# Optimization experiments

Hardware: AMD Instinct MI355X
Metric: run time of the kernel (lower is better)

Reference implementation:

```python
import jax, jax.numpy as jnp
import numpy as np

B, L, D, H, W = 32, 1024, 512, 8, 5  # batch, seq, d_model, heads, local_context_length
DK = D // H


def _local_mix(x, W0, b0, w):
    """Sliding-window local-context weighting (faithful to the torch loop version).
    Pads front with w-1 zeros, applies linear (so padded rows become the bias),
    softmax-weights each length-w causal window against the current position,
    and sums the window.  x: [B, L, D] -> [B, L, D]."""
    Bb, Ll, Dd = x.shape
    xp = jnp.pad(x, ((0, 0), (w - 1, 0), (0, 0)))          # [B, L+w-1, D]
    xp = xp @ W0 + b0                                       # linear AFTER pad (padded rows = bias)
    idx = jnp.arange(Ll)[:, None] + jnp.arange(w)[None, :]  # [L, w] window indices into padded seq
    win = xp[:, idx, :]                                     # [B, L, w, D]
    cur = xp[:, w - 1:, :]                                  # [B, L, D] current positions
    scores = jnp.einsum('bld,blwd->blw', cur, win) / jnp.sqrt(jnp.float32(Dd))
    wts = jax.nn.softmax(scores, axis=-1)                   # [B, L, w]
    return jnp.einsum('blw,blwd->bld', wts, win)            # [B, L, D]


def setup_inputs() -> dict:
    rng = jax.random.key(0)
    ks = jax.random.split(rng, 7)
    s = 0.02
    return {
        'query': jax.random.normal(ks[0], (B, L, D), jnp.float32),
        'key':   jax.random.normal(ks[1], (B, L, D), jnp.float32),
        'value': jax.random.normal(ks[2], (B, L, D), jnp.float32),
        'W0':    jax.random.normal(ks[3], (D, D), jnp.float32) * s,
        'b0':    jax.random.normal(ks[4], (D,), jnp.float32) * s,
        'Wout':  jax.random.normal(ks[5], (D, D), jnp.float32) * s,
        'bout':  jax.random.normal(ks[6], (D,), jnp.float32) * s,
    }


def reference(query, key, value, W0, b0, Wout, bout):
    q = _local_mix(query, W0, b0, W).reshape(B, L, H, DK).transpose(0, 2, 1, 3)  # [B,H,L,dk]
    k = _local_mix(key, W0, b0, W).reshape(B, L, H, DK).transpose(0, 2, 1, 3)
    v = (value @ W0 + b0).reshape(B, L, H, DK).transpose(0, 2, 1, 3)
    scores = jnp.einsum('bhqd,bhkd->bhqk', q, k) / jnp.sqrt(jnp.float32(DK))     # [B,H,L,L]
    p = jax.nn.softmax(scores, axis=-1)
    x = jnp.einsum('bhqk,bhkd->bhqd', p, v)
    x = x.transpose(0, 2, 1, 3).reshape(B, L, D)
    return x @ Wout + bout
```

## Files before the change

kernel.cpp:

```cpp
#include <hip/hip_runtime.h>


typedef __attribute__((ext_vector_type(8))) short bf16x8;
typedef __attribute__((ext_vector_type(4))) float f32x4;

#define MFMA16(a, b, c) __builtin_amdgcn_mfma_f32_16x16x32_bf16((a), (b), (c), 0, 0, 0)

static __device__ __forceinline__ float bf2f(unsigned short u) {
  union { unsigned int i; float f; } v; v.i = ((unsigned int)u) << 16; return v.f;
}
static __device__ __forceinline__ unsigned short f2b(float f) {
  union { float fv; unsigned int i; } v; v.fv = f;
  unsigned int u = v.i;
  return (unsigned short)((u + 0x7fffu + ((u >> 16) & 1u)) >> 16);
}
static __device__ __forceinline__ unsigned int cvtpk(float lo, float hi) {
  unsigned int r;
  asm("v_cvt_pk_bf16_f32 %0, %1, %2" : "=v"(r) : "v"(lo), "v"(hi));
  return r;
}
static __device__ __forceinline__ void glds16(const void* g, void* l) {
  __builtin_amdgcn_global_load_lds(
      (const __attribute__((address_space(1))) unsigned int*)g,
      (__attribute__((address_space(3))) unsigned int*)l, 16, 0, 0);
}

__global__ __launch_bounds__(256) void tcast2_k(const float* __restrict__ s0,
                                                unsigned short* __restrict__ d0,
                                                const float* __restrict__ s1,
                                                unsigned short* __restrict__ d1) {
  int i = blockIdx.x * 256 + threadIdx.x;
  const float* s = s0;
  unsigned short* d = d0;
  if (i >= 262144) { i -= 262144; s = s1; d = d1; }
  int k = i >> 9, n = i & 511;
  d[(size_t)n * 512 + k] = f2b(s[(size_t)k * 512 + n]);
}

template <int AMODE, int OUTMODE>
__device__ __forceinline__ void gemm_body(const void* __restrict__ A_,
                                          const unsigned short* __restrict__ BT,
                                          const float* __restrict__ bias,
                                          void* __restrict__ out_, int bm, int bn) {
  constexpr int TSZ = (AMODE == 0) ? 16384 : 8192;
  __shared__ __align__(16) char As[2][TSZ];
  const int tid = threadIdx.x;
  const int w = tid >> 6, l = tid & 63;
  const int lg = l >> 4, lr = l & 15;
  const int wr = w >> 1, wc = w & 1;
  const int rowbase = bm * 128;
  const int colbase = bn * 128 + wc * 64;

  f32x4 acc[4][4];
#pragma unroll
  for (int m = 0; m < 4; ++m)
#pragma unroll
    for (int n = 0; n < 4; ++n) acc[m][n] = (f32x4){0.f, 0.f, 0.f, 0.f};

  auto stage = [&](int kt, int buf) {
    if constexpr (AMODE == 0) {
      const float* Af = (const float*)A_;
#pragma unroll
      for (int j = 0; j < 4; ++j) {
        const int rb = w * 32 + j * 8;
        const int r = rb + (l >> 3);
        const int gsrc = (l & 7) ^ (r & 7);
        glds16(Af + (size_t)(rowbase + r) * 512 + kt * 32 + gsrc * 4,
               &As[buf][rb * 128]);
      }
    } else {
      const unsigned short* Ab = (const unsigned short*)A_;
#pragma unroll
      for (int j = 0; j < 2; ++j) {
        const int rb = w * 32 + j * 16;
        const int r = rb + (l >> 2);
        const int gsrc = (l & 3) ^ (r & 3) ^ ((r >> 2) & 3);
        glds16(Ab + (size_t)(rowbase + r) * 512 + kt * 32 + gsrc * 8,
               &As[buf][rb * 64]);
      }
    }
  };

  stage(0, 0);
  __syncthreads();

  for (int kt = 0; kt < 16; ++kt) {
    const int cur = kt & 1;
    bf16x8 bf[4];
#pragma unroll
    for (int n = 0; n < 4; ++n)
      bf[n] = *(const bf16x8*)(BT + (size_t)(colbase + n * 16 + lr) * 512 + kt * 32 + lg * 8);
    if (kt < 15) stage(kt + 1, cur ^ 1);
    bf16x8 af[4];
#pragma unroll
    for (int m = 0; m < 4; ++m) {
      const int r = wr * 64 + m * 16 + lr;
      if constexpr (AMODE == 0) {
        const char* Ro = &As[cur][r * 128];
        const int x = r & 7;
        const float4 a0 = *(const float4*)(Ro + ((((2 * lg) ^ x)) << 4));
        const float4 a1 = *(const float4*)(Ro + ((((2 * lg + 1) ^ x)) << 4));
        union { uint4 d; bf16x8 v; } u;
        u.d.x = cvtpk(a0.x, a0.y); u.d.y = cvtpk(a0.z, a0.w);
        u.d.z = cvtpk(a1.x, a1.y); u.d.w = cvtpk(a1.z, a1.w);
        af[m] = u.v;
      } else {
        const int gsw = lg ^ (r & 3) ^ ((r >> 2) & 3);
        af[m] = *(const bf16x8*)(&As[cur][r * 64 + (gsw << 4)]);
      }
    }
    __builtin_amdgcn_s_setprio(1);
#pragma unroll
    for (int m = 0; m < 4; ++m)
#pragma unroll
      for (int n = 0; n < 4; ++n) acc[m][n] = MFMA16(af[m], bf[n], acc[m][n]);
    __builtin_amdgcn_s_setprio(0);
    __syncthreads();
  }

#pragma unroll
  for (int m = 0; m < 4; ++m)
#pragma unroll
    for (int n = 0; n < 4; ++n) {
      const int grow0 = rowbase + wr * 64 + m * 16 + 4 * lg;
      const int gcol = colbase + n * 16 + lr;
      const float bs = bias[gcol];
#pragma unroll
      for (int r = 0; r < 4; ++r) {
        float v = acc[m][n][r] + bs;
        if constexpr (OUTMODE == 0)
          ((unsigned short*)out_)[(size_t)(grow0 + r) * 512 + gcol] = f2b(v);
        else
          ((float*)out_)[(size_t)(grow0 + r) * 512 + gcol] = v;
      }
    }
}

__global__ __launch_bounds__(256) void proj3_k(const float* __restrict__ q,
                                               const float* __restrict__ k,
                                               const float* __restrict__ v,
                                               const unsigned short* __restrict__ W0T,
                                               const float* __restrict__ b0,
                                               unsigned short* __restrict__ Pq,
                                               unsigned short* __restrict__ Pk,
                                               unsigned short* __restrict__ Pv) {
  const int wg = (blockIdx.x & 7) * 384 + (blockIdx.x >> 3);
  const int t = wg >> 10, rem = wg & 1023;
  const float* A = t == 0 ? q : t == 1 ? k : v;
  unsigned short* O = t == 0 ? Pq : t == 1 ? Pk : Pv;
  gemm_body<0, 0>(A, W0T, b0, O, rem >> 2, rem & 3);
}

__global__ __launch_bounds__(256) void gemmout_k(const unsigned short* __restrict__ A,
                                                 const unsigned short* __restrict__ WoT,
                                                 const float* __restrict__ bout,
                                                 float* __restrict__ out) {
  const int wg = (blockIdx.x & 7) * 128 + (blockIdx.x >> 3);
  gemm_body<1, 1>(A, WoT, bout, out, wg >> 2, wg & 3);
}

__global__ __launch_bounds__(256) void localmix2_k(const unsigned short* __restrict__ Pq,
                                                   const unsigned short* __restrict__ Pk,
                                                   const float* __restrict__ b0,
                                                   unsigned short* __restrict__ Qm,
                                                   unsigned short* __restrict__ Km) {
  const int w = threadIdx.x >> 6, lane = threadIdx.x & 63;
  const int pp = blockIdx.x * 4 + w;
  const unsigned short* P;
  unsigned short* out;
  float outscale;
  int p;
  if (pp < 32768) { P = Pq; out = Qm; outscale = 0.18033688011112042f; p = pp; }
  else            { P = Pk; out = Km; outscale = 1.0f; p = pp - 32768; }
  const int l = p & 1023;
  const int d0 = lane * 8;

  float win[5][8];
#pragma unroll
  for (int j = 0; j < 5; ++j) {
    const int src = l - 4 + j;
    if (src >= 0) {
      const uint4 v = *(const uint4*)(P + (size_t)(p - 4 + j) * 512 + d0);
      const unsigned short* u = (const unsigned short*)&v;
#pragma unroll
      for (int i = 0; i < 8; ++i) win[j][i] = bf2f(u[i]);
    } else {
      const float4 f0 = *(const float4*)(b0 + d0);
      const float4 f1 = *(const float4*)(b0 + d0 + 4);
      win[j][0] = f0.x; win[j][1] = f0.y; win[j][2] = f0.z; win[j][3] = f0.w;
      win[j][4] = f1.x; win[j][5] = f1.y; win[j][6] = f1.z; win[j][7] = f1.w;
    }
  }
  float s[5];
#pragma unroll
  for (int j = 0; j < 5; ++j) {
    float t = 0.f;
#pragma unroll
    for (int i = 0; i < 8; ++i) t += win[4][i] * win[j][i];
    s[j] = t;
  }
#pragma unroll
  for (int off = 1; off < 64; off <<= 1)
#pragma unroll
    for (int j = 0; j < 5; ++j) s[j] += __shfl_xor(s[j], off, 64);
  const float sc = 0.04419417382415922f;
  float mx = -1e30f;
#pragma unroll
  for (int j = 0; j < 5; ++j) { s[j] *= sc; mx = fmaxf(mx, s[j]); }
  float e[5], sum = 0.f;
#pragma unroll
  for (int j = 0; j < 5; ++j) { e[j] = __expf(s[j] - mx); sum += e[j]; }
  const float inv = 1.f / sum;
  __attribute__((ext_vector_type(8))) unsigned short o;
#pragma unroll
  for (int i = 0; i < 8; ++i) {
    float a = 0.f;
#pragma unroll
    for (int j = 0; j < 5; ++j) a += e[j] * win[j][i];
    o[i] = f2b(a * inv * outscale);
  }
  *(__attribute__((ext_vector_type(8))) unsigned short*)(out + (size_t)p * 512 + d0) = o;
}

__global__ __launch_bounds__(256) void attn_k(const unsigned short* __restrict__ Q,
                                              const unsigned short* __restrict__ K,
                                              const unsigned short* __restrict__ V,
                                              unsigned short* __restrict__ AO) {
  __shared__ unsigned short Ks[2][64 * 64];
  __shared__ unsigned short Vt[2][64 * 64];
  const int tid = threadIdx.x;
  const int w = tid >> 6, l = tid & 63;
  const int lg = l >> 4, lr = l & 15;
  const int wg = (blockIdx.x & 7) * 256 + (blockIdx.x >> 3);
  const int qt = wg & 7, bh = wg >> 3;
  const int h = bh & 7, b = bh >> 3;
  const size_t base = (size_t)(b * 1024) * 512 + h * 64;
  const unsigned short* Qb = Q + base + (size_t)(qt * 128) * 512;
  const unsigned short* Kb = K + base;
  const unsigned short* Vb = V + base;

  bf16x8 qf[2][2];
#pragma unroll
  for (int rb = 0; rb < 2; ++rb)
#pragma unroll
    for (int ks = 0; ks < 2; ++ks)
      qf[rb][ks] = *(const bf16x8*)(Qb + (size_t)(w * 32 + rb * 16 + lr) * 512 + ks * 32 + lg * 8);

  f32x4 acc[2][4];
#pragma unroll
  for (int rb = 0; rb < 2; ++rb)
#pragma unroll
    for (int nb = 0; nb < 4; ++nb) acc[rb][nb] = (f32x4){0.f, 0.f, 0.f, 0.f};
  float lrun[2] = {0.f, 0.f};

  const int sk_row = tid >> 2, sk_seg = tid & 3;
  const int sv_key = tid & 63, sv_d0 = (tid >> 6) * 16;
  const int vpos = (sv_key & 32) + ((sv_key >> 2) & 3) * 8 + ((sv_key >> 4) & 1) * 4 + (sv_key & 3);
  const int vpg = vpos >> 3, vpw = vpos & 7;
  const int r7 = sk_row & 7;

  uint4 kr0, kr1, vr0, vr1;
  auto loadT = [&](int t) {
    const uint4* ksrc = (const uint4*)(Kb + (size_t)(t * 64 + sk_row) * 512 + sk_seg * 16);
    kr0 = ksrc[0]; kr1 = ksrc[1];
    const uint4* vsrc = (const uint4*)(Vb + (size_t)(t * 64 + sv_key) * 512 + sv_d0);
    vr0 = vsrc[0]; vr1 = vsrc[1];
  };
  auto writeT = [&](int bufi) {
    unsigned short* kd = Ks[bufi];
    unsigned short* vd = Vt[bufi];
    *(uint4*)&kd[sk_row * 64 + (((2 * sk_seg) ^ r7) << 3)] = kr0;
    *(uint4*)&kd[sk_row * 64 + (((2 * sk_seg + 1) ^ r7) << 3)] = kr1;
    const unsigned short* u0 = (const unsigned short*)&vr0;
    const unsigned short* u1 = (const unsigned short*)&vr1;
#pragma unroll
    for (int j = 0; j < 8; ++j) {
      vd[(sv_d0 + j) * 64 + (((vpg ^ j) << 3) | vpw)] = u0[j];
      vd[(sv_d0 + 8 + j) * 64 + (((vpg ^ j) << 3) | vpw)] = u1[j];
    }
  };

  loadT(0);
  writeT(0);
  loadT(1);
  __syncthreads();

  const int swz0 = (lg ^ (lr & 7)) << 3, swz1 = ((4 + lg) ^ (lr & 7)) << 3;

  for (int it = 0; it < 16; ++it) {
    const int cur = it & 1;
    f32x4 sf[2][4];
    __builtin_amdgcn_s_setprio(1);
#pragma unroll
    for (int kb = 0; kb < 4; ++kb) {
      const int krow = (kb * 16 + lr) * 64;
      bf16x8 kf0 = *(const bf16x8*)&Ks[cur][krow + swz0];
      bf16x8 kf1 = *(const bf16x8*)&Ks[cur][krow + swz1];
#pragma unroll
      for (int rb = 0; rb < 2; ++rb) {
        f32x4 z = (f32x4){0.f, 0.f, 0.f, 0.f};
        z = MFMA16(kf0, qf[rb][0], z);
        z = MFMA16(kf1, qf[rb][1], z);
        sf[rb][kb] = z;
      }
    }
    __builtin_amdgcn_s_setprio(0);

    if (it < 15) writeT((it + 1) & 1);
    if (it < 14) loadT(it + 2);

#pragma unroll
    for (int rb = 0; rb < 2; ++rb) {
#pragma unroll
      for (int kb = 0; kb < 4; ++kb)
#pragma unroll
        for (int r = 0; r < 4; ++r)
          sf[rb][kb][r] = __builtin_amdgcn_exp2f(sf[rb][kb][r]);
      float s0 = (sf[rb][0][0] + sf[rb][0][1]) + (sf[rb][0][2] + sf[rb][0][3]);
      float s1 = (sf[rb][1][0] + sf[rb][1][1]) + (sf[rb][1][2] + sf[rb][1][3]);
      float s2 = (sf[rb][2][0] + sf[rb][2][1]) + (sf[rb][2][2] + sf[rb][2][3]);
      float s3 = (sf[rb][3][0] + sf[rb][3][1]) + (sf[rb][3][2] + sf[rb][3][3]);
      float t = (s0 + s1) + (s2 + s3);
      t += __shfl_xor(t, 16, 64);
      t += __shfl_xor(t, 32, 64);
      lrun[rb] += t;
    }

    union { uint4 d; bf16x8 v; } pa[2][2];
#pragma unroll
    for (int rb = 0; rb < 2; ++rb)
#pragma unroll
      for (int t2 = 0; t2 < 2; ++t2) {
        pa[rb][t2].d.x = cvtpk(sf[rb][2 * t2][0], sf[rb][2 * t2][1]);
        pa[rb][t2].d.y = cvtpk(sf[rb][2 * t2][2], sf[rb][2 * t2][3]);
        pa[rb][t2].d.z = cvtpk(sf[rb][2 * t2 + 1][0], sf[rb][2 * t2 + 1][1]);
        pa[rb][t2].d.w = cvtpk(sf[rb][2 * t2 + 1][2], sf[rb][2 * t2 + 1][3]);
      }

    __builtin_amdgcn_s_setprio(1);
#pragma unroll
    for (int t2 = 0; t2 < 2; ++t2) {
      bf16x8 vf[4];
#pragma unroll
      for (int nb = 0; nb < 4; ++nb) {
        const int vrow = (nb * 16 + lr) * 64;
        vf[nb] = *(const bf16x8*)&Vt[cur][vrow + (((4 * t2 + lg) ^ (lr & 7)) << 3)];
      }
#pragma unroll
      for (int rb = 0; rb < 2; ++rb)
#pragma unroll
        for (int nb = 0; nb < 4; ++nb) acc[rb][nb] = MFMA16(pa[rb][t2].v, vf[nb], acc[rb][nb]);
    }
    __builtin_amdgcn_s_setprio(0);
    if (it < 15) __syncthreads();
  }

#pragma unroll
  for (int rb = 0; rb < 2; ++rb) {
    const float rec = 1.f / lrun[rb];
    float lv[4];
#pragma unroll
    for (int r = 0; r < 4; ++r) lv[r] = __shfl(rec, lg * 4 + r, 64);
#pragma unroll
    for (int nb = 0; nb < 4; ++nb) {
      const int gcol = nb * 16 + lr;
#pragma unroll
      for (int r = 0; r < 4; ++r) {
        const int grow = qt * 128 + w * 32 + rb * 16 + 4 * lg + r;
        AO[base + (size_t)grow * 512 + gcol] = f2b(acc[rb][nb][r] * lv[r]);
      }
    }
  }
}

extern "C" void kernel_launch(void* const* d_in, const int* in_sizes, int n_in,
                              void* d_out, int out_size, void* d_ws, size_t ws_size,
                              hipStream_t stream) {
  const float* query = (const float*)d_in[0];
  const float* key   = (const float*)d_in[1];
  const float* value = (const float*)d_in[2];
  const float* W0    = (const float*)d_in[3];
  const float* b0    = (const float*)d_in[4];
  const float* Wout  = (const float*)d_in[5];
  const float* bout  = (const float*)d_in[6];
  float* out = (float*)d_out;

  char* ws = (char*)d_ws;
  const size_t PSZ = (size_t)32768 * 512 * 2;
  unsigned short* Pq  = (unsigned short*)(ws);
  unsigned short* Pk  = (unsigned short*)(ws + PSZ);
  unsigned short* Pv  = (unsigned short*)(ws + 2 * PSZ);
  unsigned short* Qm  = (unsigned short*)(ws + 3 * PSZ);
  unsigned short* Km  = (unsigned short*)(ws + 4 * PSZ);
  unsigned short* W0T = (unsigned short*)(ws + 5 * PSZ);
  unsigned short* WoT = (unsigned short*)(ws + 5 * PSZ + 524288);

  tcast2_k<<<2048, 256, 0, stream>>>(W0, W0T, Wout, WoT);
  proj3_k<<<3072, 256, 0, stream>>>(query, key, value, W0T, b0, Pq, Pk, Pv);
  localmix2_k<<<16384, 256, 0, stream>>>(Pq, Pk, b0, Qm, Km);
  attn_k<<<2048, 256, 0, stream>>>(Qm, Km, Pv, Pq );
  gemmout_k<<<1024, 256, 0, stream>>>(Pq, WoT, bout, out);
}
```

Measured before the change: 339.1 us.

## Triple-buffer GEMM A tiles and prefetch B fragments with manual waitcnt barriers

The projection GEMM moves from double to triple-buffered LDS staging of A tiles, issuing loads two k-steps ahead. B fragments are prefetched one step ahead into a register double buffer. Full __syncthreads are replaced with raw s_barrier plus explicit vmcnt/lgkmcnt waits so in-flight global loads are not drained every iteration. This also applies to the attention kernel's loop barriers. The intent is to hide global load latency, at the cost of more LDS and registers. There is also a risk of races if the hand-placed waitcnts do not cover every outstanding async LDS write.

After: 347.8 us. 1.03x slower.

```diff
diff --git a/kernel.cpp b/kernel.cpp
--- a/kernel.cpp
+++ b/kernel.cpp
@@ -5,6 +5,7 @@
 typedef __attribute__((ext_vector_type(4))) float f32x4;
 
 #define MFMA16(a, b, c) __builtin_amdgcn_mfma_f32_16x16x32_bf16((a), (b), (c), 0, 0, 0)
+#define CFENCE() asm volatile("" ::: "memory")
 
 static __device__ __forceinline__ float bf2f(unsigned short u) {
   union { unsigned int i; float f; } v; v.i = ((unsigned int)u) << 16; return v.f;
@@ -43,7 +44,7 @@
                                           const float* __restrict__ bias,
                                           void* __restrict__ out_, int bm, int bn) {
   constexpr int TSZ = (AMODE == 0) ? 16384 : 8192;
-  __shared__ __align__(16) char As[2][TSZ];
+  __shared__ __align__(16) char As[3][TSZ];
   const int tid = threadIdx.x;
   const int w = tid >> 6, l = tid & 63;
   const int lg = l >> 4, lr = l & 15;
@@ -80,23 +81,34 @@
       }
     }
   };
+  bf16x8 breg[2][4];
+  auto loadB = [&](int kt, int slot) {
+#pragma unroll
+    for (int n = 0; n < 4; ++n)
+      breg[slot][n] = *(const bf16x8*)(BT + (size_t)(colbase + n * 16 + lr) * 512 + kt * 32 + lg * 8);
+  };
 
   stage(0, 0);
-  __syncthreads();
-
+  stage(1, 1);
+  CFENCE();
+  loadB(0, 0);
+  CFENCE();
+  if constexpr (AMODE == 0) asm volatile("s_waitcnt vmcnt(8)" ::: "memory");
+  else                      asm volatile("s_waitcnt vmcnt(6)" ::: "memory");
+  __builtin_amdgcn_s_barrier();
+  CFENCE();
+
+#pragma unroll
   for (int kt = 0; kt < 16; ++kt) {
-    const int cur = kt & 1;
-    bf16x8 bf[4];
-#pragma unroll
-    for (int n = 0; n < 4; ++n)
-      bf[n] = *(const bf16x8*)(BT + (size_t)(colbase + n * 16 + lr) * 512 + kt * 32 + lg * 8);
-    if (kt < 15) stage(kt + 1, cur ^ 1);
+    if (kt < 14) stage(kt + 2, (kt + 2) % 3);
+    CFENCE();
+    if (kt < 15) loadB(kt + 1, (kt + 1) & 1);
     bf16x8 af[4];
 #pragma unroll
     for (int m = 0; m < 4; ++m) {
       const int r = wr * 64 + m * 16 + lr;
       if constexpr (AMODE == 0) {
-        const char* Ro = &As[cur][r * 128];
+        const char* Ro = &As[kt % 3][r * 128];
         const int x = r & 7;
         const float4 a0 = *(const float4*)(Ro + ((((2 * lg) ^ x)) << 4));
         const float4 a1 = *(const float4*)(Ro + ((((2 * lg + 1) ^ x)) << 4));
@@ -106,16 +118,20 @@
         af[m] = u.v;
       } else {
         const int gsw = lg ^ (r & 3) ^ ((r >> 2) & 3);
-        af[m] = *(const bf16x8*)(&As[cur][r * 64 + (gsw << 4)]);
+        af[m] = *(const bf16x8*)(&As[kt % 3][r * 64 + (gsw << 4)]);
       }
     }
     __builtin_amdgcn_s_setprio(1);
 #pragma unroll
     for (int m = 0; m < 4; ++m)
 #pragma unroll
-      for (int n = 0; n < 4; ++n) acc[m][n] = MFMA16(af[m], bf[n], acc[m][n]);
+      for (int n = 0; n < 4; ++n) acc[m][n] = MFMA16(af[m], breg[kt & 1][n], acc[m][n]);
     __builtin_amdgcn_s_setprio(0);
-    __syncthreads();
+    if (kt < 15) {
+      CFENCE();
+      __builtin_amdgcn_s_barrier();
+      CFENCE();
+    }
   }
 
 #pragma unroll
@@ -283,7 +299,9 @@
   loadT(0);
   writeT(0);
   loadT(1);
-  __syncthreads();
+  asm volatile("s_waitcnt lgkmcnt(0)" ::: "memory");
+  __builtin_amdgcn_s_barrier();
+  CFENCE();
 
   const int swz0 = (lg ^ (lr & 7)) << 3, swz1 = ((4 + lg) ^ (lr & 7)) << 3;
 
@@ -352,7 +370,11 @@
         for (int nb = 0; nb < 4; ++nb) acc[rb][nb] = MFMA16(pa[rb][t2].v, vf[nb], acc[rb][nb]);
     }
     __builtin_amdgcn_s_setprio(0);
-    if (it < 15) __syncthreads();
+    if (it < 15) {
+      CFENCE();
+      __builtin_amdgcn_s_barrier();
+      CFENCE();
+    }
   }
 
 #pragma unroll
```

## Stage GEMM A and B tiles through registers into LDS with prefetch pipeline

Applied to the files above, without the earlier changes.

The GEMM no longer loads A directly into LDS with global_load_lds and reads B straight from global memory per k-step. A and B tiles now go through registers into swizzled bf16 LDS buffers, with a two-deep register prefetch for A and one-step for B. Fp32 A is converted to bf16 once at staging time instead of on each LDS read. Barriers become a custom lgkmcnt wait plus s_barrier, also in the attention kernel, and the k-loop is fully unrolled. The changes aim to cut redundant global B traffic and conversion work, at the cost of higher register pressure.

After: 317.2 us. -6.5%, faster.

```diff
diff --git a/kernel.cpp b/kernel.cpp
--- a/kernel.cpp
+++ b/kernel.cpp
@@ -19,10 +19,10 @@
   asm("v_cvt_pk_bf16_f32 %0, %1, %2" : "=v"(r) : "v"(lo), "v"(hi));
   return r;
 }
-static __device__ __forceinline__ void glds16(const void* g, void* l) {
-  __builtin_amdgcn_global_load_lds(
-      (const __attribute__((address_space(1))) unsigned int*)g,
-      (__attribute__((address_space(3))) unsigned int*)l, 16, 0, 0);
+static __device__ __forceinline__ void barrier_lgkm() {
+  asm volatile("s_waitcnt lgkmcnt(0)" ::: "memory");
+  __builtin_amdgcn_s_barrier();
+  __builtin_amdgcn_sched_barrier(0);
 }
 
 __global__ __launch_bounds__(256) void tcast2_k(const float* __restrict__ s0,
@@ -42,14 +42,20 @@
                                           const unsigned short* __restrict__ BT,
                                           const float* __restrict__ bias,
                                           void* __restrict__ out_, int bm, int bn) {
-  constexpr int TSZ = (AMODE == 0) ? 16384 : 8192;
-  __shared__ __align__(16) char As[2][TSZ];
+  __shared__ unsigned short As[2][128 * 32];
+  __shared__ unsigned short Bs[2][128 * 32];
   const int tid = threadIdx.x;
   const int w = tid >> 6, l = tid & 63;
   const int lg = l >> 4, lr = l & 15;
   const int wr = w >> 1, wc = w & 1;
   const int rowbase = bm * 128;
-  const int colbase = bn * 128 + wc * 64;
+  const int colbase0 = bn * 128;
+  const int colbase = colbase0 + wc * 64;
+
+  const int srow = w * 32 + (l >> 1);
+  const int ks = l & 1;
+  const int sswz = (l >> 2) & 3;
+  const int p0 = (2 * ks) ^ sswz, p1 = (2 * ks + 1) ^ sswz;
 
   f32x4 acc[4][4];
 #pragma unroll
@@ -57,57 +63,68 @@
 #pragma unroll
     for (int n = 0; n < 4; ++n) acc[m][n] = (f32x4){0.f, 0.f, 0.f, 0.f};
 
-  auto stage = [&](int kt, int buf) {
-    if constexpr (AMODE == 0) {
-      const float* Af = (const float*)A_;
-#pragma unroll
-      for (int j = 0; j < 4; ++j) {
-        const int rb = w * 32 + j * 8;
-        const int r = rb + (l >> 3);
-        const int gsrc = (l & 7) ^ (r & 7);
-        glds16(Af + (size_t)(rowbase + r) * 512 + kt * 32 + gsrc * 4,
-               &As[buf][rb * 128]);
-      }
-    } else {
-      const unsigned short* Ab = (const unsigned short*)A_;
-#pragma unroll
-      for (int j = 0; j < 2; ++j) {
-        const int rb = w * 32 + j * 16;
-        const int r = rb + (l >> 2);
-        const int gsrc = (l & 3) ^ (r & 3) ^ ((r >> 2) & 3);
-        glds16(Ab + (size_t)(rowbase + r) * 512 + kt * 32 + gsrc * 8,
-               &As[buf][rb * 64]);
-      }
-    }
-  };
-
-  stage(0, 0);
-  __syncthreads();
-
+  float4 fa0[4], fa1[4];
+  uint4 ba0[2], ba1[2];
+  uint4 bb[2];
+
+  auto loadAf = [&](int kt, float4* d) {
+    const float* p = (const float*)A_ + (size_t)(rowbase + srow) * 512 + kt * 32 + ks * 16;
+    d[0] = ((const float4*)p)[0]; d[1] = ((const float4*)p)[1];
+    d[2] = ((const float4*)p)[2]; d[3] = ((const float4*)p)[3];
+  };
+  auto loadAb = [&](int kt, uint4* d) {
+    const unsigned short* p = (const unsigned short*)A_ + (size_t)(rowbase + srow) * 512 + kt * 32 + ks * 16;
+    d[0] = ((const uint4*)p)[0]; d[1] = ((const uint4*)p)[1];
+  };
+  auto loadB = [&](int kt) {
+    const unsigned short* p = BT + (size_t)(colbase0 + srow) * 512 + kt * 32 + ks * 16;
+    bb[0] = ((const uint4*)p)[0]; bb[1] = ((const uint4*)p)[1];
+  };
+  auto writeAf = [&](int buf, const float4* d) {
+    uint4 u0, u1;
+    u0.x = cvtpk(d[0].x, d[0].y); u0.y = cvtpk(d[0].z, d[0].w);
+    u0.z = cvtpk(d[1].x, d[1].y); u0.w = cvtpk(d[1].z, d[1].w);
+    u1.x = cvtpk(d[2].x, d[2].y); u1.y = cvtpk(d[2].z, d[2].w);
+    u1.z = cvtpk(d[3].x, d[3].y); u1.w = cvtpk(d[3].z, d[3].w);
+    *(uint4*)&As[buf][srow * 32 + p0 * 8] = u0;
+    *(uint4*)&As[buf][srow * 32 + p1 * 8] = u1;
+  };
+  auto writeAb = [&](int buf, const uint4* d) {
+    *(uint4*)&As[buf][srow * 32 + p0 * 8] = d[0];
+    *(uint4*)&As[buf][srow * 32 + p1 * 8] = d[1];
+  };
+  auto writeB = [&](int buf) {
+    *(uint4*)&Bs[buf][srow * 32 + p0 * 8] = bb[0];
+    *(uint4*)&Bs[buf][srow * 32 + p1 * 8] = bb[1];
+  };
+
+  if constexpr (AMODE == 0) { loadAf(0, fa0); } else { loadAb(0, ba0); }
+  loadB(0);
+  if constexpr (AMODE == 0) writeAf(0, fa0); else writeAb(0, ba0);
+  writeB(0);
+  if constexpr (AMODE == 0) { loadAf(1, fa1); } else { loadAb(1, ba1); }
+  barrier_lgkm();
+
+  const int rsw = ((lr >> 1) & 3);
+
+#pragma unroll
   for (int kt = 0; kt < 16; ++kt) {
     const int cur = kt & 1;
-    bf16x8 bf[4];
-#pragma unroll
-    for (int n = 0; n < 4; ++n)
-      bf[n] = *(const bf16x8*)(BT + (size_t)(colbase + n * 16 + lr) * 512 + kt * 32 + lg * 8);
-    if (kt < 15) stage(kt + 1, cur ^ 1);
-    bf16x8 af[4];
+    bf16x8 af[4], bf[4];
 #pragma unroll
     for (int m = 0; m < 4; ++m) {
       const int r = wr * 64 + m * 16 + lr;
-      if constexpr (AMODE == 0) {
-        const char* Ro = &As[cur][r * 128];
-        const int x = r & 7;
-        const float4 a0 = *(const float4*)(Ro + ((((2 * lg) ^ x)) << 4));
-        const float4 a1 = *(const float4*)(Ro + ((((2 * lg + 1) ^ x)) << 4));
-        union { uint4 d; bf16x8 v; } u;
-        u.d.x = cvtpk(a0.x, a0.y); u.d.y = cvtpk(a0.z, a0.w);
-        u.d.z = cvtpk(a1.x, a1.y); u.d.w = cvtpk(a1.z, a1.w);
-        af[m] = u.v;
-      } else {
-        const int gsw = lg ^ (r & 3) ^ ((r >> 2) & 3);
-        af[m] = *(const bf16x8*)(&As[cur][r * 64 + (gsw << 4)]);
-      }
+      af[m] = *(const bf16x8*)&As[cur][r * 32 + ((lg ^ rsw) << 3)];
+    }
+#pragma unroll
+    for (int n = 0; n < 4; ++n) {
+      const int c = wc * 64 + n * 16 + lr;
+      bf[n] = *(const bf16x8*)&Bs[cur][c * 32 + ((lg ^ rsw) << 3)];
+    }
+    if (kt < 15) loadB(kt + 1);
+    if (kt < 14) {
+      if constexpr (AMODE == 0) { if (cur == 0) loadAf(kt + 2, fa0); else loadAf(kt + 2, fa1); }
+      else                      { if (cur == 0) loadAb(kt + 2, ba0); else loadAb(kt + 2, ba1); }
     }
     __builtin_amdgcn_s_setprio(1);
 #pragma unroll
@@ -115,7 +132,12 @@
 #pragma unroll
       for (int n = 0; n < 4; ++n) acc[m][n] = MFMA16(af[m], bf[n], acc[m][n]);
     __builtin_amdgcn_s_setprio(0);
-    __syncthreads();
+    if (kt < 15) {
+      if constexpr (AMODE == 0) { if (cur == 0) writeAf(1, fa1); else writeAf(0, fa0); }
+      else                      { if (cur == 0) writeAb(1, ba1); else writeAb(0, ba0); }
+      writeB(cur ^ 1);
+      barrier_lgkm();
+    }
   }
 
 #pragma unroll
@@ -283,7 +305,7 @@
   loadT(0);
   writeT(0);
   loadT(1);
-  __syncthreads();
+  barrier_lgkm();
 
   const int swz0 = (lg ^ (lr & 7)) << 3, swz1 = ((4 + lg) ^ (lr & 7)) << 3;
 
@@ -352,7 +374,7 @@
         for (int nb = 0; nb < 4; ++nb) acc[rb][nb] = MFMA16(pa[rb][t2].v, vf[nb], acc[rb][nb]);
     }
     __builtin_amdgcn_s_setprio(0);
-    if (it < 15) __syncthreads();
+    if (it < 15) barrier_lgkm();
   }
 
 #pragma unroll
```
